# Optimization experiments

Hardware: AMD Instinct MI355X
Metric: run time of the kernel (lower is better)

## Reference

```python
import jax, jax.numpy as jnp
import numpy as np
from functools import partial

NUM_CLASSES = 80
NUM_GRID = 32
NUM_BBOX = 2
IMG_H, IMG_W = 448.0, 448.0
IOU_THRESH = 0.5
SCORE_THRESH = 0.1
N_BATCH = 128


def setup_inputs() -> dict:
    key = jax.random.key(0)
    G2 = NUM_GRID * NUM_GRID
    feat = G2 * (NUM_CLASSES + 5 * NUM_BBOX)
    x = jax.random.uniform(key, (N_BATCH, feat), dtype=jnp.float32)
    return {"x": x}


def _decode(bb):
    # bb: [G2, 5] -> [G2, 5] as (x0, y0, x1, y1, conf) in image pixels
    G = NUM_GRID
    idx = jnp.arange(G * G)
    xg = (idx % G).astype(bb.dtype)   # x varies fastest (repeat(G,1).flatten())
    yg = (idx // G).astype(bb.dtype)  # y repeated per row (repeat(1,G).flatten())
    cx = (bb[:, 0] + xg) / G
    cy = (bb[:, 1] + yg) / G
    x0 = (cx - bb[:, 2] / 2) * IMG_W
    y0 = (cy - bb[:, 3] / 2) * IMG_H
    x1 = (cx + bb[:, 2] / 2) * IMG_W
    y1 = (cy + bb[:, 3] / 2) * IMG_H
    return jnp.stack([x0, y0, x1, y1, bb[:, 4]], axis=1)


def _pairwise_iou(boxes):
    # boxes: [M, 4] -> iou [M, M]
    area = jnp.maximum(boxes[:, 2] - boxes[:, 0], 0.0) * jnp.maximum(boxes[:, 3] - boxes[:, 1], 0.0)
    lt = jnp.maximum(boxes[:, None, :2], boxes[None, :, :2])
    rb = jnp.minimum(boxes[:, None, 2:], boxes[None, :, 2:])
    wh = jnp.maximum(rb - lt, 0.0)
    inter = wh[..., 0] * wh[..., 1]
    union = area[:, None] + area[None, :] - inter
    return inter / jnp.maximum(union, 1e-9)


def _nms_keep(iou, valid_sorted, thresh):
    # greedy NMS over score-sorted boxes; suppress j>i when iou[i,j] > thresh
    M = iou.shape[0]
    j = jnp.arange(M)

    def body(i, keep):
        sup = keep[i] & (iou[i] > thresh) & (j > i)
        return keep & ~sup

    return jax.lax.fori_loop(0, M, body, valid_sorted)


def _per_image(logits, bb):
    # logits: [G2, C], bb: [G2, 5]
    probs = jax.nn.softmax(logits, axis=-1)
    dec = _decode(bb)                      # [G2, 5]
    scores = dec[:, 4]
    reserve = scores > SCORE_THRESH        # bool mask (torch filters; we mask)
    # clip boxes to image
    boxes = jnp.stack([
        jnp.clip(dec[:, 0], 0.0, IMG_W),
        jnp.clip(dec[:, 1], 0.0, IMG_H),
        jnp.clip(dec[:, 2], 0.0, IMG_W),
        jnp.clip(dec[:, 3], 0.0, IMG_H),
    ], axis=1)
    labels = jnp.argmax(probs, axis=-1)
    # batched NMS via per-class coordinate offsets (torchvision trick)
    max_coord = jnp.max(jnp.where(reserve[:, None], boxes, 0.0))
    obox = boxes + (labels.astype(boxes.dtype) * (max_coord + 1.0))[:, None]
    eff = jnp.where(reserve, scores, -1.0)
    order = jnp.argsort(-eff)
    iou = _pairwise_iou(obox[order])       # [G2, G2]
    keep_sorted = _nms_keep(iou, reserve[order], IOU_THRESH)
    keep = jnp.zeros_like(reserve).at[order].set(keep_sorted)
    return boxes, scores, reserve, keep


def reference(x):
    N = x.shape[0]
    G2 = NUM_GRID * NUM_GRID
    x = x.reshape(N, G2, NUM_CLASSES + 5 * NUM_BBOX)
    class_logits = x[..., :NUM_CLASSES]                       # [N, G2, C]
    yb = x[..., NUM_CLASSES:].reshape(N, G2, NUM_BBOX, 5)
    best = jnp.argmax(yb[..., 4], axis=-1)                    # [N, G2]
    yolo_bboxes = jnp.take_along_axis(yb, best[..., None, None], axis=2)[:, :, 0, :]  # [N, G2, 5]
    boxes, scores, reserve_mask, keep_mask = jax.vmap(_per_image)(class_logits, yolo_bboxes)
    return class_logits, yolo_bboxes, boxes, scores, reserve_mask, keep_mask
```

## Files before the change

kernel.cpp:

```cpp
#include <hip/hip_runtime.h>
#include <stdint.h>

#define NB 128
#define G 32
#define G2 1024
#define NC 80
#define IMGW 448.0f
#define NCELL (NB * G2)

#define WS_KEY_OFF  0u
#define WS_BMAX_OFF 0x100000u

__global__ __launch_bounds__(256) void percell_kernel(
    const float* __restrict__ x,
    float* __restrict__ out0, float* __restrict__ out1,
    float* __restrict__ out2, float* __restrict__ out3,
    float* __restrict__ out4, float* __restrict__ out5,
    unsigned long long* __restrict__ ws_key, float* __restrict__ ws_bmax)
{
#pragma clang fp contract(off)
    __shared__ float s_out1[16 * 5];
    __shared__ float4 s_out2[16];
    __shared__ float s_out3[16];
    __shared__ float s_out4[16];
    __shared__ unsigned long long s_key[16];
    __shared__ float s_mx[16];

    const int t = threadIdx.x;
    const int lane = t & 15;
    const int grp  = t >> 4;
    const int l64  = t & 63;
    const int base = l64 & 48;
    const int cell = blockIdx.x * 16 + grp;

    const float2* p2 = (const float2*)x + (size_t)cell * 45;
    float2* o0 = (float2*)out0 + (size_t)cell * 40;

    float bv = -INFINITY;
    int bi = 0;

    float2 a = p2[lane];
    o0[lane] = a;
    if (a.x > bv) { bv = a.x; bi = 2 * lane; }
    if (a.y > bv) { bv = a.y; bi = 2 * lane + 1; }
    float2 bq = p2[lane + 16];
    o0[lane + 16] = bq;
    if (bq.x > bv) { bv = bq.x; bi = 32 + 2 * lane; }
    if (bq.y > bv) { bv = bq.y; bi = 32 + 2 * lane + 1; }
    float2 cq = make_float2(0.0f, 0.0f);
    if (lane < 13) cq = p2[lane + 32];
    if (lane < 8) {
        o0[lane + 32] = cq;
        if (cq.x > bv) { bv = cq.x; bi = 64 + 2 * lane; }
        if (cq.y > bv) { bv = cq.y; bi = 64 + 2 * lane + 1; }
    }

#pragma unroll
    for (int o = 1; o < 16; o <<= 1) {
        float ov = __shfl_xor(bv, o, 64);
        int   oi = __shfl_xor(bi, o, 64);
        if (ov > bv || (ov == bv && oi < bi)) { bv = ov; bi = oi; }
    }

    float f40x = __shfl(cq.x, base + 8, 64),  f40y = __shfl(cq.y, base + 8, 64);
    float f41x = __shfl(cq.x, base + 9, 64),  f41y = __shfl(cq.y, base + 9, 64);
    float f42x = __shfl(cq.x, base + 10, 64), f42y = __shfl(cq.y, base + 10, 64);
    float f43x = __shfl(cq.x, base + 11, 64), f43y = __shfl(cq.y, base + 11, 64);
    float f44x = __shfl(cq.x, base + 12, 64), f44y = __shfl(cq.y, base + 12, 64);

    if (lane == 0) {
        float b0, b1, b2, b3, b4;
        if (f44y > f42x) { b0 = f42y; b1 = f43x; b2 = f43y; b3 = f44x; b4 = f44y; }
        else             { b0 = f40x; b1 = f40y; b2 = f41x; b3 = f41y; b4 = f42x; }

        s_out1[grp * 5 + 0] = b0; s_out1[grp * 5 + 1] = b1;
        s_out1[grp * 5 + 2] = b2; s_out1[grp * 5 + 3] = b3;
        s_out1[grp * 5 + 4] = b4;

        int g = cell & (G2 - 1);
        float xg = (float)(g & (G - 1));
        float yg = (float)(g >> 5);
        float cx = (b0 + xg) / 32.0f;
        float cy = (b1 + yg) / 32.0f;
        float hw = b2 / 2.0f, hh = b3 / 2.0f;
        float x0 = fminf(fmaxf((cx - hw) * IMGW, 0.0f), IMGW);
        float y0 = fminf(fmaxf((cy - hh) * IMGW, 0.0f), IMGW);
        float x1 = fminf(fmaxf((cx + hw) * IMGW, 0.0f), IMGW);
        float y1 = fminf(fmaxf((cy + hh) * IMGW, 0.0f), IMGW);

        s_out2[grp] = make_float4(x0, y0, x1, y1);
        s_out3[grp] = b4;
        bool res = b4 > 0.1f;
        s_out4[grp] = res ? 1.0f : 0.0f;

        s_key[grp] = res
            ? (((unsigned long long)bi << 41) |
               ((unsigned long long)__float_as_uint(b4) << 10) |
               (unsigned)(1023 - g))
            : (127ull << 41);
        s_mx[grp] = res ? fmaxf(fmaxf(x0, y0), fmaxf(x1, y1)) : 0.0f;
    }
    __syncthreads();

    if (t < 80)                 out1[(size_t)blockIdx.x * 80 + t] = s_out1[t];
    else if (t >= 80 && t < 96) out3[(size_t)blockIdx.x * 16 + (t - 80)] = s_out3[t - 80];
    else if (t < 112)           out4[(size_t)blockIdx.x * 16 + (t - 96)] = s_out4[t - 96];
    else if (t < 128)           ws_key[(size_t)blockIdx.x * 16 + (t - 112)] = s_key[t - 112];
    else if (t < 144)           ((float4*)out2)[(size_t)blockIdx.x * 16 + (t - 128)] = s_out2[t - 128];
    else if (t < 160)           out5[(size_t)blockIdx.x * 16 + (t - 144)] = 0.0f;
    else if (t == 160) {
        float mm = s_mx[0];
#pragma unroll
        for (int i = 1; i < 16; ++i) mm = fmaxf(mm, s_mx[i]);
        ws_bmax[blockIdx.x] = mm;
    }
}

__global__ __launch_bounds__(256) void nms_kernel(
    const unsigned long long* __restrict__ ws_key,
    const float* __restrict__ ws_bmax,
    const float4* __restrict__ boxes,
    float* __restrict__ out5)
{
#pragma clang fp contract(off)
    __shared__ unsigned long long k_s[4][64];
    __shared__ float4 ob_s[4][64];
    __shared__ float  ar_s[4][64];

    const int wv = threadIdx.x >> 6;
    const int l  = threadIdx.x & 63;
    const int w  = blockIdx.x * 4 + wv;
    const int n  = w / NC;
    const int c  = w - n * NC;

    float m = ws_bmax[n * 64 + l];
#pragma unroll
    for (int o = 32; o > 0; o >>= 1) m = fmaxf(m, __shfl_xor(m, o, 64));
    const float mult = m + 1.0f;
    const float off = (float)c * mult;

    const unsigned long long* kp = ws_key + (size_t)n * G2;
    int cnt = 0;
#pragma unroll 4
    for (int rnd = 0; rnd < 16; ++rnd) {
        unsigned long long k = kp[rnd * 64 + l];
        bool hit = (int)(k >> 41) == c;
        unsigned long long bal = __ballot(hit);
        if (hit) {
            int pos = cnt + __popcll(bal & ((1ull << l) - 1ull));
            if (pos < 64) k_s[wv][pos] = k;
        }
        cnt += __popcll(bal);
    }
    if (cnt == 0) return;
    cnt = min(cnt, 64);
    asm volatile("s_waitcnt lgkmcnt(0)" ::: "memory");

    const bool valid = l < cnt;
    const unsigned long long key = valid ? k_s[wv][l] : 0ull;
    int idx = 0;
    float4 mob = make_float4(0.f, 0.f, 0.f, 0.f);
    float marea = 0.f;
    if (valid) {
        idx = 1023 - (int)(key & 1023u);
        float4 bb = boxes[(size_t)n * G2 + idx];
        mob = make_float4(bb.x + off, bb.y + off, bb.z + off, bb.w + off);
        marea = fmaxf(mob.z - mob.x, 0.0f) * fmaxf(mob.w - mob.y, 0.0f);
    }

    int r = 0;
    for (int i = 0; i < cnt; ++i) r += (k_s[wv][i] > key);

    if (valid) { ob_s[wv][r] = mob; ar_s[wv][r] = marea; }
    asm volatile("s_waitcnt lgkmcnt(0)" ::: "memory");

    unsigned long long sup = 0;
    for (int i = 0; i < cnt; ++i) {
        float4 A = ob_s[wv][i];
        float aA = ar_s[wv][i];
        float ltx = fmaxf(A.x, mob.x);
        float lty = fmaxf(A.y, mob.y);
        float rbx = fminf(A.z, mob.z);
        float rby = fminf(A.w, mob.w);
        float ww = fmaxf(rbx - ltx, 0.0f);
        float hh = fmaxf(rby - lty, 0.0f);
        float inter = ww * hh;
        float uni = (aA + marea) - inter;
        float iou = inter / fmaxf(uni, 1e-9f);
        if (i < r && iou > 0.5f) sup |= 1ull << i;
    }

    unsigned long long kept = 0;
    for (int i = 0; i < cnt; ++i) {
        bool ki = (r == i) && ((sup & kept) == 0ull);
        kept |= __ballot(ki) ? (1ull << i) : 0ull;
    }
    if (valid) out5[(size_t)n * G2 + idx] = ((kept >> r) & 1ull) ? 1.0f : 0.0f;
}

extern "C" void kernel_launch(void* const* d_in, const int* in_sizes, int n_in,
                              void* d_out, int out_size, void* d_ws, size_t ws_size,
                              hipStream_t stream) {
    const float* x = (const float*)d_in[0];
    float* out = (float*)d_out;
    float* out0 = out;
    float* out1 = out0 + (size_t)NCELL * NC;
    float* out2 = out1 + (size_t)NCELL * 5;
    float* out3 = out2 + (size_t)NCELL * 4;
    float* out4 = out3 + (size_t)NCELL;
    float* out5 = out4 + (size_t)NCELL;

    unsigned long long* ws_key = (unsigned long long*)((char*)d_ws + WS_KEY_OFF);
    float* ws_bmax = (float*)((char*)d_ws + WS_BMAX_OFF);

    percell_kernel<<<NCELL / 16, 256, 0, stream>>>(
        x, out0, out1, out2, out3, out4, out5, ws_key, ws_bmax);
    nms_kernel<<<(NB * NC) / 4, 256, 0, stream>>>(
        ws_key, ws_bmax, (const float4*)out2, out5);
}
```

Measured before the change: 45.64 us.

## Bucket reserved boxes per class with atomics instead of scanning all keys in NMS

The per-cell kernel now appends each reserved box's score/index key into a per-(image,class) 64-slot segment using an atomic counter. The NMS kernel reads only its own segment and count instead of scanning all 1024 keys of the image with a ballot compaction. This removes the heavy redundant key scanning across 80 classes. In exchange it adds a memset launch and global atomics, and segment order becomes nondeterministic when more than 64 boxes fall in one class.

```diff
diff --git a/kernel.cpp b/kernel.cpp
--- a/kernel.cpp
+++ b/kernel.cpp
@@ -8,22 +8,23 @@
 #define IMGW 448.0f
 #define NCELL (NB * G2)
 
-#define WS_KEY_OFF  0u
-#define WS_BMAX_OFF 0x100000u
+#define WS_CNT_OFF  0u
+#define WS_BMAX_OFF 0xA000u
+#define WS_SEG_OFF  0x20000u
 
 __global__ __launch_bounds__(256) void percell_kernel(
     const float* __restrict__ x,
     float* __restrict__ out0, float* __restrict__ out1,
     float* __restrict__ out2, float* __restrict__ out3,
     float* __restrict__ out4, float* __restrict__ out5,
-    unsigned long long* __restrict__ ws_key, float* __restrict__ ws_bmax)
+    int* __restrict__ ws_cnt, float* __restrict__ ws_bmax,
+    unsigned long long* __restrict__ ws_seg)
 {
 #pragma clang fp contract(off)
     __shared__ float s_out1[16 * 5];
     __shared__ float4 s_out2[16];
     __shared__ float s_out3[16];
     __shared__ float s_out4[16];
-    __shared__ unsigned long long s_key[16];
     __shared__ float s_mx[16];
 
     const int t = threadIdx.x;
@@ -92,23 +93,25 @@
         s_out3[grp] = b4;
         bool res = b4 > 0.1f;
         s_out4[grp] = res ? 1.0f : 0.0f;
-
-        s_key[grp] = res
-            ? (((unsigned long long)bi << 41) |
-               ((unsigned long long)__float_as_uint(b4) << 10) |
-               (unsigned)(1023 - g))
-            : (127ull << 41);
         s_mx[grp] = res ? fmaxf(fmaxf(x0, y0), fmaxf(x1, y1)) : 0.0f;
+
+        if (res) {
+            int ci = (cell >> 10) * NC + bi;
+            int slot = atomicAdd(&ws_cnt[ci], 1);
+            if (slot < 64)
+                ws_seg[((size_t)ci << 6) + slot] =
+                    ((unsigned long long)__float_as_uint(b4) << 10) |
+                    (unsigned)(1023 - g);
+        }
     }
     __syncthreads();
 
     if (t < 80)                 out1[(size_t)blockIdx.x * 80 + t] = s_out1[t];
     else if (t >= 80 && t < 96) out3[(size_t)blockIdx.x * 16 + (t - 80)] = s_out3[t - 80];
     else if (t < 112)           out4[(size_t)blockIdx.x * 16 + (t - 96)] = s_out4[t - 96];
-    else if (t < 128)           ws_key[(size_t)blockIdx.x * 16 + (t - 112)] = s_key[t - 112];
-    else if (t < 144)           ((float4*)out2)[(size_t)blockIdx.x * 16 + (t - 128)] = s_out2[t - 128];
-    else if (t < 160)           out5[(size_t)blockIdx.x * 16 + (t - 144)] = 0.0f;
-    else if (t == 160) {
+    else if (t < 128)           ((float4*)out2)[(size_t)blockIdx.x * 16 + (t - 112)] = s_out2[t - 112];
+    else if (t < 144)           out5[(size_t)blockIdx.x * 16 + (t - 128)] = 0.0f;
+    else if (t == 144) {
         float mm = s_mx[0];
 #pragma unroll
         for (int i = 1; i < 16; ++i) mm = fmaxf(mm, s_mx[i]);
@@ -117,7 +120,8 @@
 }
 
 __global__ __launch_bounds__(256) void nms_kernel(
-    const unsigned long long* __restrict__ ws_key,
+    const unsigned long long* __restrict__ ws_seg,
+    const int* __restrict__ ws_cnt,
     const float* __restrict__ ws_bmax,
     const float4* __restrict__ boxes,
     float* __restrict__ out5)
@@ -133,40 +137,29 @@
     const int n  = w / NC;
     const int c  = w - n * NC;
 
+    const int cnt = min(ws_cnt[w], 64);
+    if (cnt == 0) return;
+
     float m = ws_bmax[n * 64 + l];
 #pragma unroll
     for (int o = 32; o > 0; o >>= 1) m = fmaxf(m, __shfl_xor(m, o, 64));
     const float mult = m + 1.0f;
     const float off = (float)c * mult;
 
-    const unsigned long long* kp = ws_key + (size_t)n * G2;
-    int cnt = 0;
-#pragma unroll 4
-    for (int rnd = 0; rnd < 16; ++rnd) {
-        unsigned long long k = kp[rnd * 64 + l];
-        bool hit = (int)(k >> 41) == c;
-        unsigned long long bal = __ballot(hit);
-        if (hit) {
-            int pos = cnt + __popcll(bal & ((1ull << l) - 1ull));
-            if (pos < 64) k_s[wv][pos] = k;
-        }
-        cnt += __popcll(bal);
-    }
-    if (cnt == 0) return;
-    cnt = min(cnt, 64);
-    asm volatile("s_waitcnt lgkmcnt(0)" ::: "memory");
-
     const bool valid = l < cnt;
-    const unsigned long long key = valid ? k_s[wv][l] : 0ull;
+    unsigned long long key = 0;
     int idx = 0;
     float4 mob = make_float4(0.f, 0.f, 0.f, 0.f);
     float marea = 0.f;
     if (valid) {
+        key = ws_seg[((size_t)w << 6) + l];
+        k_s[wv][l] = key;
         idx = 1023 - (int)(key & 1023u);
         float4 bb = boxes[(size_t)n * G2 + idx];
         mob = make_float4(bb.x + off, bb.y + off, bb.z + off, bb.w + off);
         marea = fmaxf(mob.z - mob.x, 0.0f) * fmaxf(mob.w - mob.y, 0.0f);
     }
+    asm volatile("s_waitcnt lgkmcnt(0)" ::: "memory");
 
     int r = 0;
     for (int i = 0; i < cnt; ++i) r += (k_s[wv][i] > key);
@@ -210,11 +203,14 @@
     float* out4 = out3 + (size_t)NCELL;
     float* out5 = out4 + (size_t)NCELL;
 
-    unsigned long long* ws_key = (unsigned long long*)((char*)d_ws + WS_KEY_OFF);
+    int* ws_cnt = (int*)((char*)d_ws + WS_CNT_OFF);
     float* ws_bmax = (float*)((char*)d_ws + WS_BMAX_OFF);
-
+    unsigned long long* ws_seg =
+        (unsigned long long*)((char*)d_ws + WS_SEG_OFF);
+
+    hipMemsetAsync(ws_cnt, 0, NB * NC * sizeof(int), stream);
     percell_kernel<<<NCELL / 16, 256, 0, stream>>>(
-        x, out0, out1, out2, out3, out4, out5, ws_key, ws_bmax);
+        x, out0, out1, out2, out3, out4, out5, ws_cnt, ws_bmax, ws_seg);
     nms_kernel<<<(NB * NC) / 4, 256, 0, stream>>>(
-        ws_key, ws_bmax, (const float4*)out2, out5);
+        ws_seg, ws_cnt, ws_bmax, (const float4*)out2, out5);
 }
```

Result: slower. 53.19 us (+16.5%).
